# Optimization experiments

Measured on AMD Instinct MI355X. Metric: run time of the kernel, lower is better.

The kernel has to match this reference:

```python
import jax, jax.numpy as jnp
import numpy as np

B, C_IN, N = 32, 64, 128
OUT_FEATS = (64, 64, 128)
ATT_DIM = 64
EPS = 1e-5  # torch BatchNorm default


def _bn(x, g, b, m, v):
    # eval-mode BatchNorm over channel axis 1 (running stats m, v)
    shape = (1, -1) + (1,) * (x.ndim - 2)
    inv = g / jnp.sqrt(v + EPS)
    return (x - m.reshape(shape)) * inv.reshape(shape) + b.reshape(shape)


def setup_inputs() -> dict:
    key = jax.random.key(0)
    ks = iter(jax.random.split(key, 48))

    def w(shape, scale=0.05):
        return jax.random.normal(next(ks), shape, jnp.float32) * scale

    inp = {"features": jax.random.normal(next(ks), (B, C_IN, N), jnp.float32)}
    in_dims = (2 * C_IN, OUT_FEATS[0], OUT_FEATS[1])
    for li in range(3):
        o, ci = OUT_FEATS[li], in_dims[li]
        inp[f"w{li}"] = w((o, ci))                  # Conv2d 1x1, no bias (BN)
        inp[f"g{li}"] = 1.0 + w((o,))               # BN gamma
        inp[f"b{li}"] = w((o,))                     # BN beta
        inp[f"m{li}"] = w((o,))                     # BN running mean
        inp[f"v{li}"] = 1.0 + 0.1 * jax.random.uniform(next(ks), (o,), jnp.float32)
    inp["wa0"] = w((ATT_DIM, OUT_FEATS[-1]))        # attention conv (no bias)
    inp["ga"] = 1.0 + w((ATT_DIM,))
    inp["ba"] = w((ATT_DIM,))
    inp["ma"] = w((ATT_DIM,))
    inp["va"] = 1.0 + 0.1 * jax.random.uniform(next(ks), (ATT_DIM,), jnp.float32)
    inp["wa1"] = w((1, ATT_DIM))                    # final attention conv (bias)
    inp["ba1"] = w((1,))
    inp["wsc"] = w((OUT_FEATS[-1], C_IN))           # shortcut Conv1d (no bias)
    inp["gsc"] = 1.0 + w((OUT_FEATS[-1],))
    inp["bsc"] = w((OUT_FEATS[-1],))
    inp["msc"] = w((OUT_FEATS[-1],))
    inp["vsc"] = 1.0 + 0.1 * jax.random.uniform(next(ks), (OUT_FEATS[-1],), jnp.float32)
    return inp


def reference(features, w0, g0, b0, m0, v0, w1, g1, b1, m1, v1,
              w2, g2, b2, m2, v2, wa0, ga, ba, ma, va, wa1, ba1,
              wsc, gsc, bsc, msc, vsc):
    n = features.shape[-1]
    # neighbor index table: row i lists all j != i, shape (N, N-1)
    base = jnp.broadcast_to(jnp.arange(n)[None, :], (n, n))
    idx = jnp.where(base >= jnp.arange(n)[:, None], base + 1, base)[:, :-1]
    x_i = features[:, :, :, None]                   # (B,C,N,1)
    x_j = features[:, :, idx]                       # (B,C,N,N-1) gather
    x = jnp.concatenate([jnp.broadcast_to(x_i, x_j.shape), x_j - x_i], axis=1)  # (B,2C,N,N-1)
    for w_, g_, b_, m_, v_ in ((w0, g0, b0, m0, v0), (w1, g1, b1, m1, v1), (w2, g2, b2, m2, v2)):
        x = jnp.einsum('oc,bcnk->bonk', w_, x)      # 1x1 conv
        x = jax.nn.relu(_bn(x, g_, b_, m_, v_))
    # attention pooling over neighbor axis k
    a = jax.nn.relu(_bn(jnp.einsum('oc,bcnk->bonk', wa0, x), ga, ba, ma, va))
    logits = jnp.einsum('oc,bcnk->bonk', wa1, a) + ba1.reshape(1, 1, 1, 1)
    attw = jax.nn.softmax(logits[:, 0], axis=-1)    # (B,N,N-1)
    fts = jnp.einsum('bcnk,bnk->bcn', x, attw)      # (B,C_out,N)
    # shortcut branch (in_feat != out_feats[-1])
    sc = _bn(jnp.einsum('oc,bcn->bon', wsc, features), gsc, bsc, msc, vsc)
    return jax.nn.relu(sc + fts)
```

## Files before the change

### kernel.cpp

```cpp
#include <hip/hip_runtime.h>

typedef unsigned short u16;
typedef short short8 __attribute__((ext_vector_type(8)));
typedef float floatx4 __attribute__((ext_vector_type(4)));
typedef __bf16 bf16x2 __attribute__((ext_vector_type(2)));

#define MFMA16(a, b, c) __builtin_amdgcn_mfma_f32_16x16x32_bf16((a), (b), (c), 0, 0, 0)

#define W1F_OFF   0u
#define B1F_OFF   8192u
#define W2F_OFF   8448u
#define B2F_OFF   24832u
#define WA0F_OFF  25344u
#define BAF_OFF   41728u
#define WA1F_OFF  41984u
#define BA1F_OFF  42240u
#define P_OFF     42496u
#define Q_OFF     1091072u
#define SC_OFF    2139648u
#define WS_TOTAL  4236800u

__device__ __align__(256) char g_ws[WS_TOTAL];

__device__ __forceinline__ float bits2f(unsigned u) {
  union { unsigned i; float f; } v; v.i = u; return v.f;
}
__device__ __forceinline__ unsigned f2bits(float f) {
  union { float f; unsigned i; } v; v.f = f; return v.i;
}
__device__ __forceinline__ u16 f2bf(float f) {
  return (u16)((f2bits(f) + 0x8000u) >> 16);
}
__device__ __forceinline__ unsigned pack2relu(float a, float b) {
#if __has_builtin(__builtin_amdgcn_cvt_pk_bf16_f32)
  union { bf16x2 h; unsigned u; } cv;
  cv.h = __builtin_amdgcn_cvt_pk_bf16_f32(fmaxf(a, 0.f), fmaxf(b, 0.f));
  return cv.u;
#else
  unsigned lo = (f2bits(fmaxf(a, 0.f)) + 0x8000u) >> 16;
  unsigned hi = (f2bits(fmaxf(b, 0.f)) + 0x8000u) & 0xffff0000u;
  return lo | hi;
#endif
}

__device__ __forceinline__ int sw64(int row, int col) {
  return (row << 6) + ((((col >> 3) ^ (row & 7)) << 3) | (col & 7));
}
__device__ __forceinline__ int sw128(int row, int col) {
  return (row << 7) + ((((col >> 3) ^ (row & 7)) << 3) | (col & 7));
}

__global__ __launch_bounds__(256) void k_pre(
    const float* __restrict__ feat, const float* __restrict__ w0,
    const float* __restrict__ g0, const float* __restrict__ b0, const float* __restrict__ m0, const float* __restrict__ v0,
    const float* __restrict__ w1, const float* __restrict__ g1, const float* __restrict__ b1, const float* __restrict__ m1, const float* __restrict__ v1,
    const float* __restrict__ w2, const float* __restrict__ g2, const float* __restrict__ b2, const float* __restrict__ m2, const float* __restrict__ v2,
    const float* __restrict__ wa0, const float* __restrict__ ga, const float* __restrict__ ba, const float* __restrict__ ma, const float* __restrict__ va,
    const float* __restrict__ wa1, const float* __restrict__ ba1,
    const float* __restrict__ wsc, const float* __restrict__ gsc, const float* __restrict__ bsc, const float* __restrict__ msc, const float* __restrict__ vsc)
{
  __shared__ float smem[9600];
  const int t = threadIdx.x;
  char* ws = g_ws;
  const int blk = blockIdx.x;

  if (blk == 512) {
    float* fs1 = smem; float* fs2 = smem + 64; float* fsa = smem + 192;
    if (t < 64) {
      float s;
      s = g1[t] * rsqrtf(v1[t] + 1e-5f); fs1[t] = s; ((float*)(ws + B1F_OFF))[t] = b1[t] - m1[t] * s;
      s = ga[t] * rsqrtf(va[t] + 1e-5f); fsa[t] = s; ((float*)(ws + BAF_OFF))[t] = ba[t] - ma[t] * s;
      ((float*)(ws + WA1F_OFF))[t] = wa1[t];
    }
    if (t < 128) { float s = g2[t] * rsqrtf(v2[t] + 1e-5f); fs2[t] = s; ((float*)(ws + B2F_OFF))[t] = b2[t] - m2[t] * s; }
    if (t == 0) ((float*)(ws + BA1F_OFF))[0] = ba1[0];
    __syncthreads();
    u16* W1f = (u16*)(ws + W1F_OFF);
    u16* W2f = (u16*)(ws + W2F_OFF);
    u16* Wa0f = (u16*)(ws + WA0F_OFF);
    for (int i = t; i < 4096; i += 256) W1f[i]  = f2bf(fs1[i >> 6] * w1[i]);
    for (int i = t; i < 8192; i += 256) W2f[i]  = f2bf(fs2[i >> 6] * w2[i]);
    for (int i = t; i < 8192; i += 256) Wa0f[i] = f2bf(fsa[i >> 7] * wa0[i]);
    return;
  }

  const int sub = blk & 255;
  const int b = sub >> 3, n0 = (sub & 7) << 4;
  float* Xs  = smem;
  float* Wsm = smem + 1280;

  {
    const int c = t >> 2, j = (t & 3) << 2;
    *(float4*)(Xs + c * 20 + j) = *(const float4*)(feat + b * 8192 + c * 128 + n0 + j);
  }

  if (blk < 256) {
    #pragma unroll
    for (int r = 0; r < 8; r++) {
      const int i = (r * 256 + t) * 4;
      float4 v = *(const float4*)(w0 + i);
      const int o = i >> 7, c = i & 127;
      float* d = Wsm + o * 129 + c;
      d[0] = v.x; d[1] = v.y; d[2] = v.z; d[3] = v.w;
    }
    __syncthreads();
    const int o = t & 63, nb = (t >> 6) << 2;
    const float s  = g0[o] * rsqrtf(v0[o] + 1e-5f);
    const float tt = b0[o] - m0[o] * s;
    const float* wr = Wsm + o * 129;
    float dA0=0.f,dA1=0.f,dA2=0.f,dA3=0.f,dB0=0.f,dB1=0.f,dB2=0.f,dB3=0.f;
    #pragma unroll
    for (int c = 0; c < 64; c++) {
      const float a = wr[c], e = wr[64 + c];
      const float4 x = *(const float4*)(Xs + c * 20 + nb);
      dA0 += a * x.x; dA1 += a * x.y; dA2 += a * x.z; dA3 += a * x.w;
      dB0 += e * x.x; dB1 += e * x.y; dB2 += e * x.z; dB3 += e * x.w;
    }
    float* Pp = (float*)(ws + P_OFF) + (b * 128 + n0 + nb) * 64 + o;
    float* Qp = (float*)(ws + Q_OFF) + (b * 128 + n0 + nb) * 64 + o;
    Pp[0]   = s * dB0; Pp[64]  = s * dB1; Pp[128] = s * dB2; Pp[192] = s * dB3;
    Qp[0]   = s * (dA0 - dB0) + tt; Qp[64]  = s * (dA1 - dB1) + tt;
    Qp[128] = s * (dA2 - dB2) + tt; Qp[192] = s * (dA3 - dB3) + tt;
  } else {
    #pragma unroll
    for (int r = 0; r < 8; r++) {
      const int i = (r * 256 + t) * 4;
      float4 v = *(const float4*)(wsc + i);
      const int o = i >> 6, c = i & 63;
      float* d = Wsm + o * 65 + c;
      d[0] = v.x; d[1] = v.y; d[2] = v.z; d[3] = v.w;
    }
    __syncthreads();
    const int o = t & 127, h = (t >> 7) << 3;
    const float s  = gsc[o] * rsqrtf(vsc[o] + 1e-5f);
    const float tt = bsc[o] - msc[o] * s;
    const float* wr = Wsm + o * 65;
    float d0=0.f,d1=0.f,d2=0.f,d3=0.f,d4=0.f,d5=0.f,d6=0.f,d7=0.f;
    #pragma unroll
    for (int c = 0; c < 64; c++) {
      const float a = wr[c];
      const float4 x0 = *(const float4*)(Xs + c * 20 + h);
      const float4 x1 = *(const float4*)(Xs + c * 20 + h + 4);
      d0 += a * x0.x; d1 += a * x0.y; d2 += a * x0.z; d3 += a * x0.w;
      d4 += a * x1.x; d5 += a * x1.y; d6 += a * x1.z; d7 += a * x1.w;
    }
    float* SCp = (float*)(ws + SC_OFF) + (b * 128 + n0 + h) * 128 + o;
    SCp[0]   = s * d0 + tt; SCp[128] = s * d1 + tt; SCp[256] = s * d2 + tt; SCp[384] = s * d3 + tt;
    SCp[512] = s * d4 + tt; SCp[640] = s * d5 + tt; SCp[768] = s * d6 + tt; SCp[896] = s * d7 + tt;
  }
}

__global__ __launch_bounds__(256, 4) void k_main(float* __restrict__ out)
{
  __shared__ alignas(16) u16 buf[16384];
  __shared__ float parts[4][128];
  __shared__ float attws[128];

  const int blk = blockIdx.x, b = blk >> 7, n = blk & 127, t = threadIdx.x;
  const char* ws = g_ws;
  const float* Pb  = (const float*)(ws + P_OFF);
  const float* Qb  = (const float*)(ws + Q_OFF);
  const float* SCb = (const float*)(ws + SC_OFF);
  const u16*   W1f = (const u16*)(ws + W1F_OFF);
  const float* b1f = (const float*)(ws + B1F_OFF);
  const u16*   W2f = (const u16*)(ws + W2F_OFF);
  const float* b2f = (const float*)(ws + B2F_OFF);
  const u16*   Wa0f= (const u16*)(ws + WA0F_OFF);
  const float* baf = (const float*)(ws + BAF_OFF);
  const float* wa1f= (const float*)(ws + WA1F_OFF);
  const float  ba1v= *(const float*)(ws + BA1F_OFF);

  u16* H0 = buf;
  u16* H1 = buf + 8192;
  u16* H2 = buf;

  const int lane = t & 63, wid = t >> 6, quad = lane >> 4, l16 = lane & 15;
  const int koff = quad * 8;

  const short8 a1w0 = *(const short8*)(W1f + (wid * 16 + l16) * 64 + koff);
  const short8 a1w1 = *(const short8*)(W1f + (wid * 16 + l16) * 64 + 32 + koff);
  const short8 a2w00 = *(const short8*)(W2f + (wid * 32 + l16) * 64 + koff);
  const short8 a2w01 = *(const short8*)(W2f + (wid * 32 + l16) * 64 + 32 + koff);
  const short8 a2w10 = *(const short8*)(W2f + (wid * 32 + 16 + l16) * 64 + koff);
  const short8 a2w11 = *(const short8*)(W2f + (wid * 32 + 16 + l16) * 64 + 32 + koff);

  {
    const int k = t >> 1, half = t & 1;
    const int j = (k < 127) ? ((k < n) ? k : (k + 1)) : n;
    const float4* pr = (const float4*)(Pb + ((b << 7) + j) * 64 + half * 32);
    const float4* qr = (const float4*)(Qb + blk * 64 + half * 32);
    #pragma unroll
    for (int ii = 0; ii < 4; ii++) {
      float4 p0 = pr[2 * ii],     q0 = qr[2 * ii];
      float4 p1 = pr[2 * ii + 1], q1 = qr[2 * ii + 1];
      uint4 sv;
      sv.x = pack2relu(q0.x + p0.x, q0.y + p0.y);
      sv.y = pack2relu(q0.z + p0.z, q0.w + p0.w);
      sv.z = pack2relu(q1.x + p1.x, q1.y + p1.y);
      sv.w = pack2relu(q1.z + p1.z, q1.w + p1.w);
      *(uint4*)(H0 + sw64(k, half * 32 + ii * 8)) = sv;
    }
  }
  __syncthreads();

  {
    const int rr = wid * 16 + quad * 4;
    const float4 bb = *(const float4*)(b1f + rr);
    floatx4 binit; binit[0] = bb.x; binit[1] = bb.y; binit[2] = bb.z; binit[3] = bb.w;
    floatx4 acc[8];
    #pragma unroll
    for (int et = 0; et < 8; et++) acc[et] = binit;
    #pragma unroll
    for (int et = 0; et < 8; et++) {
      const int row = et * 16 + l16;
      short8 bf0 = *(const short8*)(H0 + sw64(row, koff));
      short8 bf1 = *(const short8*)(H0 + sw64(row, koff + 32));
      acc[et] = MFMA16(a1w0, bf0, acc[et]);
      acc[et] = MFMA16(a1w1, bf1, acc[et]);
    }
    #pragma unroll
    for (int et = 0; et < 8; et++) {
      uint2 sv;
      sv.x = pack2relu(acc[et][0], acc[et][1]);
      sv.y = pack2relu(acc[et][2], acc[et][3]);
      *(uint2*)(H1 + sw64(et * 16 + l16, rr)) = sv;
    }
  }
  __syncthreads();

  {
    const int r2 = wid * 32 + quad * 4;
    const float4 bba = *(const float4*)(b2f + r2);
    const float4 bbb = *(const float4*)(b2f + r2 + 16);
    floatx4 ia; ia[0] = bba.x; ia[1] = bba.y; ia[2] = bba.z; ia[3] = bba.w;
    floatx4 ib; ib[0] = bbb.x; ib[1] = bbb.y; ib[2] = bbb.z; ib[3] = bbb.w;
    floatx4 acc[2][8];
    #pragma unroll
    for (int et = 0; et < 8; et++) { acc[0][et] = ia; acc[1][et] = ib; }
    #pragma unroll
    for (int et = 0; et < 8; et++) {
      const int row = et * 16 + l16;
      short8 bf0 = *(const short8*)(H1 + sw64(row, koff));
      short8 bf1 = *(const short8*)(H1 + sw64(row, koff + 32));
      acc[0][et] = MFMA16(a2w00, bf0, acc[0][et]);
      acc[0][et] = MFMA16(a2w01, bf1, acc[0][et]);
      acc[1][et] = MFMA16(a2w10, bf0, acc[1][et]);
      acc[1][et] = MFMA16(a2w11, bf1, acc[1][et]);
    }
    __syncthreads();
    #pragma unroll
    for (int m = 0; m < 2; m++) {
      const int rr = r2 + m * 16;
      #pragma unroll
      for (int et = 0; et < 8; et++) {
        uint2 sv;
        sv.x = pack2relu(acc[m][et][0], acc[m][et][1]);
        sv.y = pack2relu(acc[m][et][2], acc[m][et][3]);
        *(uint2*)(H2 + sw128(et * 16 + l16, rr)) = sv;
      }
    }
  }

  short8 a3[4];
  #pragma unroll
  for (int ks = 0; ks < 4; ks++)
    a3[ks] = *(const short8*)(Wa0f + (wid * 16 + l16) * 128 + ks * 32 + koff);

  __syncthreads();

  float scv = 0.f;
  if (t < 128) scv = SCb[blk * 128 + t];
  float* outp = out + ((b << 7) + (t & 127)) * 128 + n;

  {
    const int rr = wid * 16 + quad * 4;
    const float4 bb = *(const float4*)(baf + rr);
    const float4 wv = *(const float4*)(wa1f + rr);
    floatx4 binit; binit[0] = bb.x; binit[1] = bb.y; binit[2] = bb.z; binit[3] = bb.w;
    floatx4 acc[8];
    #pragma unroll
    for (int et = 0; et < 8; et++) acc[et] = binit;
    #pragma unroll
    for (int et = 0; et < 8; et++) {
      const int row = et * 16 + l16;
      #pragma unroll
      for (int ks = 0; ks < 4; ks++) {
        short8 bf = *(const short8*)(H2 + sw128(row, koff + ks * 32));
        acc[et] = MFMA16(a3[ks], bf, acc[et]);
      }
    }
    #pragma unroll
    for (int et = 0; et < 8; et++) {
      float p = wv.x * fmaxf(acc[et][0], 0.f) + wv.y * fmaxf(acc[et][1], 0.f)
              + wv.z * fmaxf(acc[et][2], 0.f) + wv.w * fmaxf(acc[et][3], 0.f);
      p += __shfl_xor(p, 16); p += __shfl_xor(p, 32);
      if (quad == 0) parts[wid][et * 16 + l16] = p;
    }
  }

  const int chg = t & 15, eg = t >> 4;
  uint4 hv[8];
  #pragma unroll
  for (int i = 0; i < 8; i++)
    hv[i] = *(const uint4*)(H2 + sw128(eg * 8 + i, chg * 8));

  __syncthreads();

  if (wid == 0) {
    float a0 = parts[0][lane] + parts[1][lane] + parts[2][lane] + parts[3][lane] + ba1v;
    float a1 = (lane == 63) ? -1e30f
             : (parts[0][lane + 64] + parts[1][lane + 64] + parts[2][lane + 64] + parts[3][lane + 64] + ba1v);
    float mx = fmaxf(a0, a1);
    #pragma unroll
    for (int off = 32; off >= 1; off >>= 1) mx = fmaxf(mx, __shfl_xor(mx, off));
    float e0 = expf(a0 - mx), e1 = expf(a1 - mx);
    float sm = e0 + e1;
    #pragma unroll
    for (int off = 32; off >= 1; off >>= 1) sm += __shfl_xor(sm, off);
    float inv = 1.f / sm;
    attws[lane] = e0 * inv;
    attws[lane + 64] = e1 * inv;
  }
  __syncthreads();

  {
    float fa[8];
    #pragma unroll
    for (int k = 0; k < 8; k++) fa[k] = 0.f;
    #pragma unroll
    for (int i = 0; i < 8; i++) {
      const float w = attws[eg * 8 + i];
      uint4 v = hv[i];
      unsigned u;
      u = v.x; fa[0] += w * bits2f(u << 16); fa[1] += w * bits2f(u & 0xffff0000u);
      u = v.y; fa[2] += w * bits2f(u << 16); fa[3] += w * bits2f(u & 0xffff0000u);
      u = v.z; fa[4] += w * bits2f(u << 16); fa[5] += w * bits2f(u & 0xffff0000u);
      u = v.w; fa[6] += w * bits2f(u << 16); fa[7] += w * bits2f(u & 0xffff0000u);
    }
    #pragma unroll
    for (int k = 0; k < 8; k++) { fa[k] += __shfl_xor(fa[k], 16); fa[k] += __shfl_xor(fa[k], 32); }
    if (lane < 16) {
      #pragma unroll
      for (int k = 0; k < 8; k++) parts[wid][chg * 8 + k] = fa[k];
    }
  }
  __syncthreads();

  if (t < 128) {
    float fts = parts[0][t] + parts[1][t] + parts[2][t] + parts[3][t];
    *outp = fmaxf(scv + fts, 0.f);
  }
}

extern "C" void kernel_launch(void* const* d_in, const int* in_sizes, int n_in,
                              void* d_out, int out_size, void* d_ws, size_t ws_size,
                              hipStream_t stream)
{
  (void)d_ws; (void)ws_size; (void)in_sizes; (void)n_in; (void)out_size;
  const float* feat = (const float*)d_in[0];
  const float *w0 = (const float*)d_in[1],  *g0 = (const float*)d_in[2],  *b0 = (const float*)d_in[3],  *m0 = (const float*)d_in[4],  *v0 = (const float*)d_in[5];
  const float *w1 = (const float*)d_in[6],  *g1 = (const float*)d_in[7],  *b1 = (const float*)d_in[8],  *m1 = (const float*)d_in[9],  *v1 = (const float*)d_in[10];
  const float *w2 = (const float*)d_in[11], *g2 = (const float*)d_in[12], *b2 = (const float*)d_in[13], *m2 = (const float*)d_in[14], *v2 = (const float*)d_in[15];
  const float *wa0= (const float*)d_in[16], *ga = (const float*)d_in[17], *ba = (const float*)d_in[18], *ma = (const float*)d_in[19], *va = (const float*)d_in[20];
  const float *wa1= (const float*)d_in[21], *ba1= (const float*)d_in[22];
  const float *wsc= (const float*)d_in[23], *gsc= (const float*)d_in[24], *bsc= (const float*)d_in[25], *msc= (const float*)d_in[26], *vsc= (const float*)d_in[27];

  k_pre<<<dim3(513), dim3(256), 0, stream>>>(
      feat, w0, g0, b0, m0, v0, w1, g1, b1, m1, v1, w2, g2, b2, m2, v2,
      wa0, ga, ba, ma, va, wa1, ba1, wsc, gsc, bsc, msc, vsc);
  k_main<<<dim3(4096), dim3(256), 0, stream>>>((float*)d_out);
}
```

Measured before the change: 168.5 us.

## Double k_main block to 512 threads, splitting neighbor rows across wave pairs

k_main now runs 8 waves per block instead of 4. Each output-channel tile is handled by two waves, each covering half of the 128 neighbor rows. This halves per-wave MFMA accumulators and per-thread pooling loads, and the final reduction sums 8 partial buffers instead of 4. The aim is more waves resident per CU to hide LDS and global latency. In exchange, block-wide barriers now span more waves, and the tighter launch-bounds target may force register caps or spills.

New measurement: 183.3 us. 1.09x slower.

```diff
diff --git a/kernel.cpp b/kernel.cpp
--- a/kernel.cpp
+++ b/kernel.cpp
@@ -150,10 +150,10 @@
   }
 }
 
-__global__ __launch_bounds__(256, 4) void k_main(float* __restrict__ out)
+__global__ __launch_bounds__(512, 6) void k_main(float* __restrict__ out)
 {
   __shared__ alignas(16) u16 buf[16384];
-  __shared__ float parts[4][128];
+  __shared__ float parts[8][128];
   __shared__ float attws[128];
 
   const int blk = blockIdx.x, b = blk >> 7, n = blk & 127, t = threadIdx.x;
@@ -176,87 +176,89 @@
 
   const int lane = t & 63, wid = t >> 6, quad = lane >> 4, l16 = lane & 15;
   const int koff = quad * 8;
-
-  const short8 a1w0 = *(const short8*)(W1f + (wid * 16 + l16) * 64 + koff);
-  const short8 a1w1 = *(const short8*)(W1f + (wid * 16 + l16) * 64 + 32 + koff);
-  const short8 a2w00 = *(const short8*)(W2f + (wid * 32 + l16) * 64 + koff);
-  const short8 a2w01 = *(const short8*)(W2f + (wid * 32 + l16) * 64 + 32 + koff);
-  const short8 a2w10 = *(const short8*)(W2f + (wid * 32 + 16 + l16) * 64 + koff);
-  const short8 a2w11 = *(const short8*)(W2f + (wid * 32 + 16 + l16) * 64 + 32 + koff);
-
-  {
-    const int k = t >> 1, half = t & 1;
+  const int mt = wid & 3, eh = wid >> 2;
+  const int c2 = mt * 32;
+
+  const short8 a1w0 = *(const short8*)(W1f + (mt * 16 + l16) * 64 + koff);
+  const short8 a1w1 = *(const short8*)(W1f + (mt * 16 + l16) * 64 + 32 + koff);
+  const short8 a2w00 = *(const short8*)(W2f + (c2 + l16) * 64 + koff);
+  const short8 a2w01 = *(const short8*)(W2f + (c2 + l16) * 64 + 32 + koff);
+  const short8 a2w10 = *(const short8*)(W2f + (c2 + 16 + l16) * 64 + koff);
+  const short8 a2w11 = *(const short8*)(W2f + (c2 + 16 + l16) * 64 + 32 + koff);
+
+  {
+    const int k = t >> 2, q4 = t & 3;
     const int j = (k < 127) ? ((k < n) ? k : (k + 1)) : n;
-    const float4* pr = (const float4*)(Pb + ((b << 7) + j) * 64 + half * 32);
-    const float4* qr = (const float4*)(Qb + blk * 64 + half * 32);
-    #pragma unroll
-    for (int ii = 0; ii < 4; ii++) {
-      float4 p0 = pr[2 * ii],     q0 = qr[2 * ii];
-      float4 p1 = pr[2 * ii + 1], q1 = qr[2 * ii + 1];
-      uint4 sv;
-      sv.x = pack2relu(q0.x + p0.x, q0.y + p0.y);
-      sv.y = pack2relu(q0.z + p0.z, q0.w + p0.w);
-      sv.z = pack2relu(q1.x + p1.x, q1.y + p1.y);
-      sv.w = pack2relu(q1.z + p1.z, q1.w + p1.w);
-      *(uint4*)(H0 + sw64(k, half * 32 + ii * 8)) = sv;
-    }
-  }
-  __syncthreads();
-
-  {
-    const int rr = wid * 16 + quad * 4;
-    const float4 bb = *(const float4*)(b1f + rr);
+    const float4* pr = (const float4*)(Pb + ((b << 7) + j) * 64 + q4 * 16);
+    const float4* qr = (const float4*)(Qb + blk * 64 + q4 * 16);
+    float4 p0 = pr[0], p1 = pr[1], p2 = pr[2], p3 = pr[3];
+    float4 q0 = qr[0], q1 = qr[1], q2 = qr[2], q3 = qr[3];
+    uint4 s0, s1;
+    s0.x = pack2relu(q0.x + p0.x, q0.y + p0.y);
+    s0.y = pack2relu(q0.z + p0.z, q0.w + p0.w);
+    s0.z = pack2relu(q1.x + p1.x, q1.y + p1.y);
+    s0.w = pack2relu(q1.z + p1.z, q1.w + p1.w);
+    s1.x = pack2relu(q2.x + p2.x, q2.y + p2.y);
+    s1.y = pack2relu(q2.z + p2.z, q2.w + p2.w);
+    s1.z = pack2relu(q3.x + p3.x, q3.y + p3.y);
+    s1.w = pack2relu(q3.z + p3.z, q3.w + p3.w);
+    *(uint4*)(H0 + sw64(k, q4 * 16))     = s0;
+    *(uint4*)(H0 + sw64(k, q4 * 16 + 8)) = s1;
+  }
+  __syncthreads();
+
+  {
+    const float4 bb = *(const float4*)(b1f + mt * 16 + quad * 4);
     floatx4 binit; binit[0] = bb.x; binit[1] = bb.y; binit[2] = bb.z; binit[3] = bb.w;
-    floatx4 acc[8];
-    #pragma unroll
-    for (int et = 0; et < 8; et++) acc[et] = binit;
-    #pragma unroll
-    for (int et = 0; et < 8; et++) {
-      const int row = et * 16 + l16;
+    floatx4 acc[4];
+    #pragma unroll
+    for (int i = 0; i < 4; i++) acc[i] = binit;
+    #pragma unroll
+    for (int i = 0; i < 4; i++) {
+      const int row = eh * 64 + i * 16 + l16;
       short8 bf0 = *(const short8*)(H0 + sw64(row, koff));
       short8 bf1 = *(const short8*)(H0 + sw64(row, koff + 32));
-      acc[et] = MFMA16(a1w0, bf0, acc[et]);
-      acc[et] = MFMA16(a1w1, bf1, acc[et]);
-    }
-    #pragma unroll
-    for (int et = 0; et < 8; et++) {
+      acc[i] = MFMA16(a1w0, bf0, acc[i]);
+      acc[i] = MFMA16(a1w1, bf1, acc[i]);
+    }
+    #pragma unroll
+    for (int i = 0; i < 4; i++) {
       uint2 sv;
-      sv.x = pack2relu(acc[et][0], acc[et][1]);
-      sv.y = pack2relu(acc[et][2], acc[et][3]);
-      *(uint2*)(H1 + sw64(et * 16 + l16, rr)) = sv;
-    }
-  }
-  __syncthreads();
-
-  {
-    const int r2 = wid * 32 + quad * 4;
-    const float4 bba = *(const float4*)(b2f + r2);
-    const float4 bbb = *(const float4*)(b2f + r2 + 16);
+      sv.x = pack2relu(acc[i][0], acc[i][1]);
+      sv.y = pack2relu(acc[i][2], acc[i][3]);
+      *(uint2*)(H1 + sw64(eh * 64 + i * 16 + l16, mt * 16 + quad * 4)) = sv;
+    }
+  }
+  __syncthreads();
+
+  {
+    const float4 bba = *(const float4*)(b2f + c2 + quad * 4);
+    const float4 bbb = *(const float4*)(b2f + c2 + 16 + quad * 4);
     floatx4 ia; ia[0] = bba.x; ia[1] = bba.y; ia[2] = bba.z; ia[3] = bba.w;
     floatx4 ib; ib[0] = bbb.x; ib[1] = bbb.y; ib[2] = bbb.z; ib[3] = bbb.w;
-    floatx4 acc[2][8];
-    #pragma unroll
-    for (int et = 0; et < 8; et++) { acc[0][et] = ia; acc[1][et] = ib; }
-    #pragma unroll
-    for (int et = 0; et < 8; et++) {
-      const int row = et * 16 + l16;
+    floatx4 acc[2][4];
+    #pragma unroll
+    for (int i = 0; i < 4; i++) { acc[0][i] = ia; acc[1][i] = ib; }
+    #pragma unroll
+    for (int i = 0; i < 4; i++) {
+      const int row = eh * 64 + i * 16 + l16;
       short8 bf0 = *(const short8*)(H1 + sw64(row, koff));
       short8 bf1 = *(const short8*)(H1 + sw64(row, koff + 32));
-      acc[0][et] = MFMA16(a2w00, bf0, acc[0][et]);
-      acc[0][et] = MFMA16(a2w01, bf1, acc[0][et]);
-      acc[1][et] = MFMA16(a2w10, bf0, acc[1][et]);
-      acc[1][et] = MFMA16(a2w11, bf1, acc[1][et]);
+      acc[0][i] = MFMA16(a2w00, bf0, acc[0][i]);
+      acc[0][i] = MFMA16(a2w01, bf1, acc[0][i]);
+      acc[1][i] = MFMA16(a2w10, bf0, acc[1][i]);
+      acc[1][i] = MFMA16(a2w11, bf1, acc[1][i]);
     }
     __syncthreads();
     #pragma unroll
     for (int m = 0; m < 2; m++) {
-      const int rr = r2 + m * 16;
+      const int cc = c2 + m * 16 + quad * 4;
       #pragma unroll
-      for (int et = 0; et < 8; et++) {
+      for (int i = 0; i < 4; i++) {
         uint2 sv;
-        sv.x = pack2relu(acc[m][et][0], acc[m][et][1]);
-        sv.y = pack2relu(acc[m][et][2], acc[m][et][3]);
-        *(uint2*)(H2 + sw128(et * 16 + l16, rr)) = sv;
+        sv.x = pack2relu(acc[m][i][0], acc[m][i][1]);
+        sv.y = pack2relu(acc[m][i][2], acc[m][i][3]);
+        *(uint2*)(H2 + sw128(eh * 64 + i * 16 + l16, cc)) = sv;
       }
     }
   }
@@ -264,7 +266,7 @@
   short8 a3[4];
   #pragma unroll
   for (int ks = 0; ks < 4; ks++)
-    a3[ks] = *(const short8*)(Wa0f + (wid * 16 + l16) * 128 + ks * 32 + koff);
+    a3[ks] = *(const short8*)(Wa0f + (mt * 16 + l16) * 128 + ks * 32 + koff);
 
   __syncthreads();
 
@@ -273,36 +275,35 @@
   float* outp = out + ((b << 7) + (t & 127)) * 128 + n;
 
   {
-    const int rr = wid * 16 + quad * 4;
-    const float4 bb = *(const float4*)(baf + rr);
-    const float4 wv = *(const float4*)(wa1f + rr);
+    const float4 bb = *(const float4*)(baf + mt * 16 + quad * 4);
+    const float4 wv = *(const float4*)(wa1f + mt * 16 + quad * 4);
     floatx4 binit; binit[0] = bb.x; binit[1] = bb.y; binit[2] = bb.z; binit[3] = bb.w;
-    floatx4 acc[8];
-    #pragma unroll
-    for (int et = 0; et < 8; et++) acc[et] = binit;
-    #pragma unroll
-    for (int et = 0; et < 8; et++) {
-      const int row = et * 16 + l16;
+    floatx4 acc[4];
+    #pragma unroll
+    for (int i = 0; i < 4; i++) acc[i] = binit;
+    #pragma unroll
+    for (int i = 0; i < 4; i++) {
+      const int row = eh * 64 + i * 16 + l16;
       #pragma unroll
       for (int ks = 0; ks < 4; ks++) {
         short8 bf = *(const short8*)(H2 + sw128(row, koff + ks * 32));
-        acc[et] = MFMA16(a3[ks], bf, acc[et]);
+        acc[i] = MFMA16(a3[ks], bf, acc[i]);
       }
     }
     #pragma unroll
-    for (int et = 0; et < 8; et++) {
-      float p = wv.x * fmaxf(acc[et][0], 0.f) + wv.y * fmaxf(acc[et][1], 0.f)
-              + wv.z * fmaxf(acc[et][2], 0.f) + wv.w * fmaxf(acc[et][3], 0.f);
+    for (int i = 0; i < 4; i++) {
+      float p = wv.x * fmaxf(acc[i][0], 0.f) + wv.y * fmaxf(acc[i][1], 0.f)
+              + wv.z * fmaxf(acc[i][2], 0.f) + wv.w * fmaxf(acc[i][3], 0.f);
       p += __shfl_xor(p, 16); p += __shfl_xor(p, 32);
-      if (quad == 0) parts[wid][et * 16 + l16] = p;
+      if (quad == 0) parts[mt][eh * 64 + i * 16 + l16] = p;
     }
   }
 
   const int chg = t & 15, eg = t >> 4;
-  uint4 hv[8];
+  uint4 hv[4];
   #pragma unroll
-  for (int i = 0; i < 8; i++)
-    hv[i] = *(const uint4*)(H2 + sw128(eg * 8 + i, chg * 8));
+  for (int i = 0; i < 4; i++)
+    hv[i] = *(const uint4*)(H2 + sw128(eg * 4 + i, chg * 8));
 
   __syncthreads();
 
@@ -328,8 +329,8 @@
     #pragma unroll
     for (int k = 0; k < 8; k++) fa[k] = 0.f;
     #pragma unroll
-    for (int i = 0; i < 8; i++) {
-      const float w = attws[eg * 8 + i];
+    for (int i = 0; i < 4; i++) {
+      const float w = attws[eg * 4 + i];
       uint4 v = hv[i];
       unsigned u;
       u = v.x; fa[0] += w * bits2f(u << 16); fa[1] += w * bits2f(u & 0xffff0000u);
@@ -347,7 +348,8 @@
   __syncthreads();
 
   if (t < 128) {
-    float fts = parts[0][t] + parts[1][t] + parts[2][t] + parts[3][t];
+    float fts = parts[0][t] + parts[1][t] + parts[2][t] + parts[3][t]
+              + parts[4][t] + parts[5][t] + parts[6][t] + parts[7][t];
     *outp = fmaxf(scv + fts, 0.f);
   }
 }
@@ -368,5 +370,5 @@
   k_pre<<<dim3(513), dim3(256), 0, stream>>>(
       feat, w0, g0, b0, m0, v0, w1, g1, b1, m1, v1, w2, g2, b2, m2, v2,
       wa0, ga, ba, ma, va, wa1, ba1, wsc, gsc, bsc, msc, vsc);
-  k_main<<<dim3(4096), dim3(256), 0, stream>>>((float*)d_out);
-}
+  k_main<<<dim3(4096), dim3(512), 0, stream>>>((float*)d_out);
+}
```

## Process two center points per block to reuse weight fragments and halve block count

Applied to the files above, without the earlier changes.

Each block of k_main now handles two consecutive n values instead of one. Every phase is doubled across both, reusing the register-held weight fragments, and the output is written as a float2. The aim is to spread per-block fixed costs (weight loads, barriers, softmax setup) over twice the work and to interleave independent MFMA chains. The cost is twice the LDS (64KB buffer), more registers, launch bounds lowered to 2 blocks per CU and half as many blocks in the grid, which reduces occupancy.

Measured after the change: 178.3 us. +5.8%, slower.

```diff
diff --git a/kernel.cpp b/kernel.cpp
--- a/kernel.cpp
+++ b/kernel.cpp
@@ -150,13 +150,13 @@
   }
 }
 
-__global__ __launch_bounds__(256, 4) void k_main(float* __restrict__ out)
+__global__ __launch_bounds__(256, 2) void k_main(float* __restrict__ out)
 {
-  __shared__ alignas(16) u16 buf[16384];
-  __shared__ float parts[4][128];
-  __shared__ float attws[128];
-
-  const int blk = blockIdx.x, b = blk >> 7, n = blk & 127, t = threadIdx.x;
+  __shared__ alignas(16) u16 buf[32768];
+  __shared__ float parts[2][4][128];
+  __shared__ float attws[2][128];
+
+  const int blk = blockIdx.x, b = blk >> 6, npair = (blk & 63) << 1, t = threadIdx.x;
   const char* ws = g_ws;
   const float* Pb  = (const float*)(ws + P_OFF);
   const float* Qb  = (const float*)(ws + Q_OFF);
@@ -170,12 +170,11 @@
   const float* wa1f= (const float*)(ws + WA1F_OFF);
   const float  ba1v= *(const float*)(ws + BA1F_OFF);
 
-  u16* H0 = buf;
-  u16* H1 = buf + 8192;
-  u16* H2 = buf;
-
   const int lane = t & 63, wid = t >> 6, quad = lane >> 4, l16 = lane & 15;
   const int koff = quad * 8;
+
+  u16* H0c[2] = { buf,        buf + 16384 };
+  u16* H1c[2] = { buf + 8192, buf + 24576 };
 
   const short8 a1w0 = *(const short8*)(W1f + (wid * 16 + l16) * 64 + koff);
   const short8 a1w1 = *(const short8*)(W1f + (wid * 16 + l16) * 64 + 32 + koff);
@@ -186,19 +185,23 @@
 
   {
     const int k = t >> 1, half = t & 1;
-    const int j = (k < 127) ? ((k < n) ? k : (k + 1)) : n;
-    const float4* pr = (const float4*)(Pb + ((b << 7) + j) * 64 + half * 32);
-    const float4* qr = (const float4*)(Qb + blk * 64 + half * 32);
-    #pragma unroll
-    for (int ii = 0; ii < 4; ii++) {
-      float4 p0 = pr[2 * ii],     q0 = qr[2 * ii];
-      float4 p1 = pr[2 * ii + 1], q1 = qr[2 * ii + 1];
-      uint4 sv;
-      sv.x = pack2relu(q0.x + p0.x, q0.y + p0.y);
-      sv.y = pack2relu(q0.z + p0.z, q0.w + p0.w);
-      sv.z = pack2relu(q1.x + p1.x, q1.y + p1.y);
-      sv.w = pack2relu(q1.z + p1.z, q1.w + p1.w);
-      *(uint4*)(H0 + sw64(k, half * 32 + ii * 8)) = sv;
+    #pragma unroll
+    for (int c = 0; c < 2; c++) {
+      const int nc = npair + c;
+      const int j = (k < 127) ? ((k < nc) ? k : (k + 1)) : nc;
+      const float4* pr = (const float4*)(Pb + ((b << 7) + j) * 64 + half * 32);
+      const float4* qr = (const float4*)(Qb + ((b << 7) + nc) * 64 + half * 32);
+      #pragma unroll
+      for (int ii = 0; ii < 4; ii++) {
+        float4 p0 = pr[2 * ii],     q0 = qr[2 * ii];
+        float4 p1 = pr[2 * ii + 1], q1 = qr[2 * ii + 1];
+        uint4 sv;
+        sv.x = pack2relu(q0.x + p0.x, q0.y + p0.y);
+        sv.y = pack2relu(q0.z + p0.z, q0.w + p0.w);
+        sv.z = pack2relu(q1.x + p1.x, q1.y + p1.y);
+        sv.w = pack2relu(q1.z + p1.z, q1.w + p1.w);
+        *(uint4*)(H0c[c] + sw64(k, half * 32 + ii * 8)) = sv;
+      }
     }
   }
   __syncthreads();
@@ -207,24 +210,32 @@
     const int rr = wid * 16 + quad * 4;
     const float4 bb = *(const float4*)(b1f + rr);
     floatx4 binit; binit[0] = bb.x; binit[1] = bb.y; binit[2] = bb.z; binit[3] = bb.w;
-    floatx4 acc[8];
-    #pragma unroll
-    for (int et = 0; et < 8; et++) acc[et] = binit;
+    floatx4 acc[2][8];
+    #pragma unroll
+    for (int c = 0; c < 2; c++)
+      #pragma unroll
+      for (int et = 0; et < 8; et++) acc[c][et] = binit;
     #pragma unroll
     for (int et = 0; et < 8; et++) {
       const int row = et * 16 + l16;
-      short8 bf0 = *(const short8*)(H0 + sw64(row, koff));
-      short8 bf1 = *(const short8*)(H0 + sw64(row, koff + 32));
-      acc[et] = MFMA16(a1w0, bf0, acc[et]);
-      acc[et] = MFMA16(a1w1, bf1, acc[et]);
-    }
-    #pragma unroll
-    for (int et = 0; et < 8; et++) {
-      uint2 sv;
-      sv.x = pack2relu(acc[et][0], acc[et][1]);
-      sv.y = pack2relu(acc[et][2], acc[et][3]);
-      *(uint2*)(H1 + sw64(et * 16 + l16, rr)) = sv;
-    }
+      short8 b00 = *(const short8*)(H0c[0] + sw64(row, koff));
+      short8 b01 = *(const short8*)(H0c[0] + sw64(row, koff + 32));
+      short8 b10 = *(const short8*)(H0c[1] + sw64(row, koff));
+      short8 b11 = *(const short8*)(H0c[1] + sw64(row, koff + 32));
+      acc[0][et] = MFMA16(a1w0, b00, acc[0][et]);
+      acc[0][et] = MFMA16(a1w1, b01, acc[0][et]);
+      acc[1][et] = MFMA16(a1w0, b10, acc[1][et]);
+      acc[1][et] = MFMA16(a1w1, b11, acc[1][et]);
+    }
+    #pragma unroll
+    for (int c = 0; c < 2; c++)
+      #pragma unroll
+      for (int et = 0; et < 8; et++) {
+        uint2 sv;
+        sv.x = pack2relu(acc[c][et][0], acc[c][et][1]);
+        sv.y = pack2relu(acc[c][et][2], acc[c][et][3]);
+        *(uint2*)(H1c[c] + sw64(et * 16 + l16, rr)) = sv;
+      }
   }
   __syncthreads();
 
@@ -234,31 +245,47 @@
     const float4 bbb = *(const float4*)(b2f + r2 + 16);
     floatx4 ia; ia[0] = bba.x; ia[1] = bba.y; ia[2] = bba.z; ia[3] = bba.w;
     floatx4 ib; ib[0] = bbb.x; ib[1] = bbb.y; ib[2] = bbb.z; ib[3] = bbb.w;
-    floatx4 acc[2][8];
-    #pragma unroll
-    for (int et = 0; et < 8; et++) { acc[0][et] = ia; acc[1][et] = ib; }
+    floatx4 acc[2][2][8];
+    #pragma unroll
+    for (int c = 0; c < 2; c++)
+      #pragma unroll
+      for (int et = 0; et < 8; et++) { acc[c][0][et] = ia; acc[c][1][et] = ib; }
     #pragma unroll
     for (int et = 0; et < 8; et++) {
       const int row = et * 16 + l16;
-      short8 bf0 = *(const short8*)(H1 + sw64(row, koff));
-      short8 bf1 = *(const short8*)(H1 + sw64(row, koff + 32));
-      acc[0][et] = MFMA16(a2w00, bf0, acc[0][et]);
-      acc[0][et] = MFMA16(a2w01, bf1, acc[0][et]);
-      acc[1][et] = MFMA16(a2w10, bf0, acc[1][et]);
-      acc[1][et] = MFMA16(a2w11, bf1, acc[1][et]);
-    }
+      short8 b00 = *(const short8*)(H1c[0] + sw64(row, koff));
+      short8 b01 = *(const short8*)(H1c[0] + sw64(row, koff + 32));
+      short8 b10 = *(const short8*)(H1c[1] + sw64(row, koff));
+      short8 b11 = *(const short8*)(H1c[1] + sw64(row, koff + 32));
+      acc[0][0][et] = MFMA16(a2w00, b00, acc[0][0][et]);
+      acc[0][0][et] = MFMA16(a2w01, b01, acc[0][0][et]);
+      acc[0][1][et] = MFMA16(a2w10, b00, acc[0][1][et]);
+      acc[0][1][et] = MFMA16(a2w11, b01, acc[0][1][et]);
+      acc[1][0][et] = MFMA16(a2w00, b10, acc[1][0][et]);
+      acc[1][0][et] = MFMA16(a2w01, b11, acc[1][0][et]);
+      acc[1][1][et] = MFMA16(a2w10, b10, acc[1][1][et]);
+      acc[1][1][et] = MFMA16(a2w11, b11, acc[1][1][et]);
+    }
+    uint2 sv[2][2][8];
+    #pragma unroll
+    for (int c = 0; c < 2; c++)
+      #pragma unroll
+      for (int m = 0; m < 2; m++)
+        #pragma unroll
+        for (int et = 0; et < 8; et++) {
+          sv[c][m][et].x = pack2relu(acc[c][m][et][0], acc[c][m][et][1]);
+          sv[c][m][et].y = pack2relu(acc[c][m][et][2], acc[c][m][et][3]);
+        }
     __syncthreads();
     #pragma unroll
-    for (int m = 0; m < 2; m++) {
-      const int rr = r2 + m * 16;
-      #pragma unroll
-      for (int et = 0; et < 8; et++) {
-        uint2 sv;
-        sv.x = pack2relu(acc[m][et][0], acc[m][et][1]);
-        sv.y = pack2relu(acc[m][et][2], acc[m][et][3]);
-        *(uint2*)(H2 + sw128(et * 16 + l16, rr)) = sv;
+    for (int c = 0; c < 2; c++)
+      #pragma unroll
+      for (int m = 0; m < 2; m++) {
+        const int cc = r2 + m * 16;
+        #pragma unroll
+        for (int et = 0; et < 8; et++)
+          *(uint2*)(H0c[c] + sw128(et * 16 + l16, cc)) = sv[c][m][et];
       }
-    }
   }
 
   short8 a3[4];
@@ -268,48 +295,59 @@
 
   __syncthreads();
 
-  float scv = 0.f;
-  if (t < 128) scv = SCb[blk * 128 + t];
-  float* outp = out + ((b << 7) + (t & 127)) * 128 + n;
+  float scv0 = 0.f, scv1 = 0.f;
+  if (t < 128) {
+    scv0 = SCb[((b << 7) + npair) * 128 + t];
+    scv1 = SCb[((b << 7) + npair + 1) * 128 + t];
+  }
 
   {
     const int rr = wid * 16 + quad * 4;
     const float4 bb = *(const float4*)(baf + rr);
     const float4 wv = *(const float4*)(wa1f + rr);
     floatx4 binit; binit[0] = bb.x; binit[1] = bb.y; binit[2] = bb.z; binit[3] = bb.w;
-    floatx4 acc[8];
-    #pragma unroll
-    for (int et = 0; et < 8; et++) acc[et] = binit;
+    floatx4 acc[2][8];
+    #pragma unroll
+    for (int c = 0; c < 2; c++)
+      #pragma unroll
+      for (int et = 0; et < 8; et++) acc[c][et] = binit;
     #pragma unroll
     for (int et = 0; et < 8; et++) {
       const int row = et * 16 + l16;
       #pragma unroll
       for (int ks = 0; ks < 4; ks++) {
-        short8 bf = *(const short8*)(H2 + sw128(row, koff + ks * 32));
-        acc[et] = MFMA16(a3[ks], bf, acc[et]);
+        short8 bf0 = *(const short8*)(H0c[0] + sw128(row, koff + ks * 32));
+        short8 bf1 = *(const short8*)(H0c[1] + sw128(row, koff + ks * 32));
+        acc[0][et] = MFMA16(a3[ks], bf0, acc[0][et]);
+        acc[1][et] = MFMA16(a3[ks], bf1, acc[1][et]);
       }
     }
     #pragma unroll
-    for (int et = 0; et < 8; et++) {
-      float p = wv.x * fmaxf(acc[et][0], 0.f) + wv.y * fmaxf(acc[et][1], 0.f)
-              + wv.z * fmaxf(acc[et][2], 0.f) + wv.w * fmaxf(acc[et][3], 0.f);
-      p += __shfl_xor(p, 16); p += __shfl_xor(p, 32);
-      if (quad == 0) parts[wid][et * 16 + l16] = p;
-    }
+    for (int c = 0; c < 2; c++)
+      #pragma unroll
+      for (int et = 0; et < 8; et++) {
+        float p = wv.x * fmaxf(acc[c][et][0], 0.f) + wv.y * fmaxf(acc[c][et][1], 0.f)
+                + wv.z * fmaxf(acc[c][et][2], 0.f) + wv.w * fmaxf(acc[c][et][3], 0.f);
+        p += __shfl_xor(p, 16); p += __shfl_xor(p, 32);
+        if (quad == 0) parts[c][wid][et * 16 + l16] = p;
+      }
   }
 
   const int chg = t & 15, eg = t >> 4;
-  uint4 hv[8];
+  uint4 hv[2][8];
   #pragma unroll
-  for (int i = 0; i < 8; i++)
-    hv[i] = *(const uint4*)(H2 + sw128(eg * 8 + i, chg * 8));
-
-  __syncthreads();
-
-  if (wid == 0) {
-    float a0 = parts[0][lane] + parts[1][lane] + parts[2][lane] + parts[3][lane] + ba1v;
+  for (int c = 0; c < 2; c++)
+    #pragma unroll
+    for (int i = 0; i < 8; i++)
+      hv[c][i] = *(const uint4*)(H0c[c] + sw128(eg * 8 + i, chg * 8));
+
+  __syncthreads();
+
+  if (wid < 2) {
+    const int c = wid;
+    float a0 = parts[c][0][lane] + parts[c][1][lane] + parts[c][2][lane] + parts[c][3][lane] + ba1v;
     float a1 = (lane == 63) ? -1e30f
-             : (parts[0][lane + 64] + parts[1][lane + 64] + parts[2][lane + 64] + parts[3][lane + 64] + ba1v);
+             : (parts[c][0][lane + 64] + parts[c][1][lane + 64] + parts[c][2][lane + 64] + parts[c][3][lane + 64] + ba1v);
     float mx = fmaxf(a0, a1);
     #pragma unroll
     for (int off = 32; off >= 1; off >>= 1) mx = fmaxf(mx, __shfl_xor(mx, off));
@@ -318,19 +356,20 @@
     #pragma unroll
     for (int off = 32; off >= 1; off >>= 1) sm += __shfl_xor(sm, off);
     float inv = 1.f / sm;
-    attws[lane] = e0 * inv;
-    attws[lane + 64] = e1 * inv;
-  }
-  __syncthreads();
-
-  {
+    attws[c][lane] = e0 * inv;
+    attws[c][lane + 64] = e1 * inv;
+  }
+  __syncthreads();
+
+  #pragma unroll
+  for (int c = 0; c < 2; c++) {
     float fa[8];
     #pragma unroll
     for (int k = 0; k < 8; k++) fa[k] = 0.f;
     #pragma unroll
     for (int i = 0; i < 8; i++) {
-      const float w = attws[eg * 8 + i];
-      uint4 v = hv[i];
+      const float w = attws[c][eg * 8 + i];
+      uint4 v = hv[c][i];
       unsigned u;
       u = v.x; fa[0] += w * bits2f(u << 16); fa[1] += w * bits2f(u & 0xffff0000u);
       u = v.y; fa[2] += w * bits2f(u << 16); fa[3] += w * bits2f(u & 0xffff0000u);
@@ -341,14 +380,18 @@
     for (int k = 0; k < 8; k++) { fa[k] += __shfl_xor(fa[k], 16); fa[k] += __shfl_xor(fa[k], 32); }
     if (lane < 16) {
       #pragma unroll
-      for (int k = 0; k < 8; k++) parts[wid][chg * 8 + k] = fa[k];
+      for (int k = 0; k < 8; k++) parts[c][wid][chg * 8 + k] = fa[k];
     }
   }
   __syncthreads();
 
   if (t < 128) {
-    float fts = parts[0][t] + parts[1][t] + parts[2][t] + parts[3][t];
-    *outp = fmaxf(scv + fts, 0.f);
+    float f0 = parts[0][0][t] + parts[0][1][t] + parts[0][2][t] + parts[0][3][t];
+    float f1 = parts[1][0][t] + parts[1][1][t] + parts[1][2][t] + parts[1][3][t];
+    float2 o;
+    o.x = fmaxf(scv0 + f0, 0.f);
+    o.y = fmaxf(scv1 + f1, 0.f);
+    *(float2*)(out + (((b << 7) + t) << 7) + npair) = o;
   }
 }
 
@@ -368,5 +411,5 @@
   k_pre<<<dim3(513), dim3(256), 0, stream>>>(
       feat, w0, g0, b0, m0, v0, w1, g1, b1, m1, v1, w2, g2, b2, m2, v2,
       wa0, ga, ba, ma, va, wa1, ba1, wsc, gsc, bsc, msc, vsc);
-  k_main<<<dim3(4096), dim3(256), 0, stream>>>((float*)d_out);
-}
+  k_main<<<dim3(2048), dim3(256), 0, stream>>>((float*)d_out);
+}
```

## Retile per-wave MFMA work to 2D channel×edge blocks and edge-split attention

Applied to the files above, without the earlier changes.

Layers 1 and 2 switch from each wave owning a channel slice across all 128 edges to a 2×2 split of channel half by edge half. Each B fragment loaded from LDS is now reused across 2 or 4 weight tiles, which cuts LDS reads per MFMA. The attention layer now splits by edge rows per wave with all 64 output channels held in registers, so the logit reduction happens within a wave and the cross-wave parts sum goes away. The cost is more registers for weight fragments (a3 grows to 16 short8, a2 to 8), which may pressure occupancy under launch_bounds(256,4).

New measurement: 197.5 us. 17.2% more time.

```diff
diff --git a/kernel.cpp b/kernel.cpp
--- a/kernel.cpp
+++ b/kernel.cpp
@@ -154,7 +154,7 @@
 {
   __shared__ alignas(16) u16 buf[16384];
   __shared__ float parts[4][128];
-  __shared__ float attws[128];
+  __shared__ float logits[128];
 
   const int blk = blockIdx.x, b = blk >> 7, n = blk & 127, t = threadIdx.x;
   const char* ws = g_ws;
@@ -176,13 +176,20 @@
 
   const int lane = t & 63, wid = t >> 6, quad = lane >> 4, l16 = lane & 15;
   const int koff = quad * 8;
-
-  const short8 a1w0 = *(const short8*)(W1f + (wid * 16 + l16) * 64 + koff);
-  const short8 a1w1 = *(const short8*)(W1f + (wid * 16 + l16) * 64 + 32 + koff);
-  const short8 a2w00 = *(const short8*)(W2f + (wid * 32 + l16) * 64 + koff);
-  const short8 a2w01 = *(const short8*)(W2f + (wid * 32 + l16) * 64 + 32 + koff);
-  const short8 a2w10 = *(const short8*)(W2f + (wid * 32 + 16 + l16) * 64 + koff);
-  const short8 a2w11 = *(const short8*)(W2f + (wid * 32 + 16 + l16) * 64 + 32 + koff);
+  const int chH = wid & 1, ehb = (wid >> 1) << 6;
+
+  short8 a1[2][2];
+  #pragma unroll
+  for (int m = 0; m < 2; m++)
+    #pragma unroll
+    for (int kk = 0; kk < 2; kk++)
+      a1[m][kk] = *(const short8*)(W1f + ((chH << 5) + m * 16 + l16) * 64 + kk * 32 + koff);
+  short8 a2[4][2];
+  #pragma unroll
+  for (int m = 0; m < 4; m++)
+    #pragma unroll
+    for (int kk = 0; kk < 2; kk++)
+      a2[m][kk] = *(const short8*)(W2f + ((chH << 6) + m * 16 + l16) * 64 + kk * 32 + koff);
 
   {
     const int k = t >> 1, half = t & 1;
@@ -204,67 +211,74 @@
   __syncthreads();
 
   {
-    const int rr = wid * 16 + quad * 4;
-    const float4 bb = *(const float4*)(b1f + rr);
-    floatx4 binit; binit[0] = bb.x; binit[1] = bb.y; binit[2] = bb.z; binit[3] = bb.w;
-    floatx4 acc[8];
-    #pragma unroll
-    for (int et = 0; et < 8; et++) acc[et] = binit;
-    #pragma unroll
-    for (int et = 0; et < 8; et++) {
-      const int row = et * 16 + l16;
+    floatx4 acc[2][4];
+    #pragma unroll
+    for (int m = 0; m < 2; m++) {
+      const float4 bb = *(const float4*)(b1f + (chH << 5) + m * 16 + quad * 4);
+      floatx4 bi; bi[0] = bb.x; bi[1] = bb.y; bi[2] = bb.z; bi[3] = bb.w;
+      #pragma unroll
+      for (int et = 0; et < 4; et++) acc[m][et] = bi;
+    }
+    #pragma unroll
+    for (int et = 0; et < 4; et++) {
+      const int row = ehb + et * 16 + l16;
       short8 bf0 = *(const short8*)(H0 + sw64(row, koff));
       short8 bf1 = *(const short8*)(H0 + sw64(row, koff + 32));
-      acc[et] = MFMA16(a1w0, bf0, acc[et]);
-      acc[et] = MFMA16(a1w1, bf1, acc[et]);
-    }
-    #pragma unroll
-    for (int et = 0; et < 8; et++) {
-      uint2 sv;
-      sv.x = pack2relu(acc[et][0], acc[et][1]);
-      sv.y = pack2relu(acc[et][2], acc[et][3]);
-      *(uint2*)(H1 + sw64(et * 16 + l16, rr)) = sv;
-    }
-  }
-  __syncthreads();
-
-  {
-    const int r2 = wid * 32 + quad * 4;
-    const float4 bba = *(const float4*)(b2f + r2);
-    const float4 bbb = *(const float4*)(b2f + r2 + 16);
-    floatx4 ia; ia[0] = bba.x; ia[1] = bba.y; ia[2] = bba.z; ia[3] = bba.w;
-    floatx4 ib; ib[0] = bbb.x; ib[1] = bbb.y; ib[2] = bbb.z; ib[3] = bbb.w;
-    floatx4 acc[2][8];
-    #pragma unroll
-    for (int et = 0; et < 8; et++) { acc[0][et] = ia; acc[1][et] = ib; }
-    #pragma unroll
-    for (int et = 0; et < 8; et++) {
-      const int row = et * 16 + l16;
-      short8 bf0 = *(const short8*)(H1 + sw64(row, koff));
-      short8 bf1 = *(const short8*)(H1 + sw64(row, koff + 32));
-      acc[0][et] = MFMA16(a2w00, bf0, acc[0][et]);
-      acc[0][et] = MFMA16(a2w01, bf1, acc[0][et]);
-      acc[1][et] = MFMA16(a2w10, bf0, acc[1][et]);
-      acc[1][et] = MFMA16(a2w11, bf1, acc[1][et]);
-    }
-    __syncthreads();
-    #pragma unroll
-    for (int m = 0; m < 2; m++) {
-      const int rr = r2 + m * 16;
-      #pragma unroll
-      for (int et = 0; et < 8; et++) {
+      acc[0][et] = MFMA16(a1[0][0], bf0, acc[0][et]);
+      acc[0][et] = MFMA16(a1[0][1], bf1, acc[0][et]);
+      acc[1][et] = MFMA16(a1[1][0], bf0, acc[1][et]);
+      acc[1][et] = MFMA16(a1[1][1], bf1, acc[1][et]);
+    }
+    #pragma unroll
+    for (int m = 0; m < 2; m++)
+      #pragma unroll
+      for (int et = 0; et < 4; et++) {
         uint2 sv;
         sv.x = pack2relu(acc[m][et][0], acc[m][et][1]);
         sv.y = pack2relu(acc[m][et][2], acc[m][et][3]);
-        *(uint2*)(H2 + sw128(et * 16 + l16, rr)) = sv;
+        *(uint2*)(H1 + sw64(ehb + et * 16 + l16, (chH << 5) + m * 16 + quad * 4)) = sv;
       }
-    }
-  }
-
-  short8 a3[4];
+  }
+  __syncthreads();
+
+  {
+    floatx4 acc[4][4];
+    #pragma unroll
+    for (int m = 0; m < 4; m++) {
+      const float4 bb = *(const float4*)(b2f + (chH << 6) + m * 16 + quad * 4);
+      floatx4 bi; bi[0] = bb.x; bi[1] = bb.y; bi[2] = bb.z; bi[3] = bb.w;
+      #pragma unroll
+      for (int et = 0; et < 4; et++) acc[m][et] = bi;
+    }
+    #pragma unroll
+    for (int et = 0; et < 4; et++) {
+      const int row = ehb + et * 16 + l16;
+      short8 bf0 = *(const short8*)(H1 + sw64(row, koff));
+      short8 bf1 = *(const short8*)(H1 + sw64(row, koff + 32));
+      #pragma unroll
+      for (int m = 0; m < 4; m++) {
+        acc[m][et] = MFMA16(a2[m][0], bf0, acc[m][et]);
+        acc[m][et] = MFMA16(a2[m][1], bf1, acc[m][et]);
+      }
+    }
+    __syncthreads();
+    #pragma unroll
+    for (int m = 0; m < 4; m++)
+      #pragma unroll
+      for (int et = 0; et < 4; et++) {
+        uint2 sv;
+        sv.x = pack2relu(acc[m][et][0], acc[m][et][1]);
+        sv.y = pack2relu(acc[m][et][2], acc[m][et][3]);
+        *(uint2*)(H2 + sw128(ehb + et * 16 + l16, (chH << 6) + m * 16 + quad * 4)) = sv;
+      }
+  }
+
+  short8 a3[4][4];
   #pragma unroll
-  for (int ks = 0; ks < 4; ks++)
-    a3[ks] = *(const short8*)(Wa0f + (wid * 16 + l16) * 128 + ks * 32 + koff);
+  for (int m = 0; m < 4; m++)
+    #pragma unroll
+    for (int ks = 0; ks < 4; ks++)
+      a3[m][ks] = *(const short8*)(Wa0f + (m * 16 + l16) * 128 + ks * 32 + koff);
 
   __syncthreads();
 
@@ -273,28 +287,27 @@
   float* outp = out + ((b << 7) + (t & 127)) * 128 + n;
 
   {
-    const int rr = wid * 16 + quad * 4;
-    const float4 bb = *(const float4*)(baf + rr);
-    const float4 wv = *(const float4*)(wa1f + rr);
-    floatx4 binit; binit[0] = bb.x; binit[1] = bb.y; binit[2] = bb.z; binit[3] = bb.w;
-    floatx4 acc[8];
-    #pragma unroll
-    for (int et = 0; et < 8; et++) acc[et] = binit;
-    #pragma unroll
-    for (int et = 0; et < 8; et++) {
-      const int row = et * 16 + l16;
-      #pragma unroll
-      for (int ks = 0; ks < 4; ks++) {
-        short8 bf = *(const short8*)(H2 + sw128(row, koff + ks * 32));
-        acc[et] = MFMA16(a3[ks], bf, acc[et]);
+    #pragma unroll
+    for (int et2 = 0; et2 < 2; et2++) {
+      const int erow = (wid << 5) + et2 * 16 + l16;
+      short8 bfr[4];
+      #pragma unroll
+      for (int ks = 0; ks < 4; ks++)
+        bfr[ks] = *(const short8*)(H2 + sw128(erow, koff + ks * 32));
+      float p = 0.f;
+      #pragma unroll
+      for (int m = 0; m < 4; m++) {
+        const float4 bb = *(const float4*)(baf + m * 16 + quad * 4);
+        const float4 wv = *(const float4*)(wa1f + m * 16 + quad * 4);
+        floatx4 ac; ac[0] = bb.x; ac[1] = bb.y; ac[2] = bb.z; ac[3] = bb.w;
+        #pragma unroll
+        for (int ks = 0; ks < 4; ks++)
+          ac = MFMA16(a3[m][ks], bfr[ks], ac);
+        p += wv.x * fmaxf(ac[0], 0.f) + wv.y * fmaxf(ac[1], 0.f)
+           + wv.z * fmaxf(ac[2], 0.f) + wv.w * fmaxf(ac[3], 0.f);
       }
-    }
-    #pragma unroll
-    for (int et = 0; et < 8; et++) {
-      float p = wv.x * fmaxf(acc[et][0], 0.f) + wv.y * fmaxf(acc[et][1], 0.f)
-              + wv.z * fmaxf(acc[et][2], 0.f) + wv.w * fmaxf(acc[et][3], 0.f);
       p += __shfl_xor(p, 16); p += __shfl_xor(p, 32);
-      if (quad == 0) parts[wid][et * 16 + l16] = p;
+      if (quad == 0) logits[erow] = p;
     }
   }
 
@@ -307,9 +320,8 @@
   __syncthreads();
 
   if (wid == 0) {
-    float a0 = parts[0][lane] + parts[1][lane] + parts[2][lane] + parts[3][lane] + ba1v;
-    float a1 = (lane == 63) ? -1e30f
-             : (parts[0][lane + 64] + parts[1][lane + 64] + parts[2][lane + 64] + parts[3][lane + 64] + ba1v);
+    float a0 = logits[lane] + ba1v;
+    float a1 = (lane == 63) ? -1e30f : (logits[lane + 64] + ba1v);
     float mx = fmaxf(a0, a1);
     #pragma unroll
     for (int off = 32; off >= 1; off >>= 1) mx = fmaxf(mx, __shfl_xor(mx, off));
@@ -318,8 +330,8 @@
     #pragma unroll
     for (int off = 32; off >= 1; off >>= 1) sm += __shfl_xor(sm, off);
     float inv = 1.f / sm;
-    attws[lane] = e0 * inv;
-    attws[lane + 64] = e1 * inv;
+    logits[lane] = e0 * inv;
+    logits[lane + 64] = e1 * inv;
   }
   __syncthreads();
 
@@ -329,7 +341,7 @@
     for (int k = 0; k < 8; k++) fa[k] = 0.f;
     #pragma unroll
     for (int i = 0; i < 8; i++) {
-      const float w = attws[eg * 8 + i];
+      const float w = logits[eg * 8 + i];
       uint4 v = hv[i];
       unsigned u;
       u = v.x; fa[0] += w * bits2f(u << 16); fa[1] += w * bits2f(u & 0xffff0000u);
```
